# Kernel tuning notes

Measured on AMD Instinct MI355X. Metric: run time of the kernel, lower is better.

Reference implementation:

```python
import jax, jax.numpy as jnp
import numpy as np
import math

B, S, D, H = 4, 2048, 1024, 16
HD = D // H  # head dim = 64


def setup_inputs() -> dict:
    key = jax.random.key(0)
    ks = jax.random.split(key, 8)
    queries = jax.random.normal(ks[0], (B, S, D), dtype=jnp.float32)
    keys = jax.random.normal(ks[1], (B, S, D), dtype=jnp.float32)
    values = jax.random.normal(ks[2], (B, S, D), dtype=jnp.float32)
    valid_lens = jnp.maximum(jax.random.randint(ks[3], (B,), 0, S), 1).astype(jnp.int64)
    scale = 1.0 / math.sqrt(D)
    Wq = jax.random.normal(ks[4], (H, D, HD), dtype=jnp.float32) * scale
    Wk = jax.random.normal(ks[5], (H, D, HD), dtype=jnp.float32) * scale
    Wv = jax.random.normal(ks[6], (H, D, HD), dtype=jnp.float32) * scale
    Wo = jax.random.normal(ks[7], (H * HD, D), dtype=jnp.float32) * scale
    return {"queries": queries, "keys": keys, "values": values,
            "valid_lens": valid_lens, "Wq": Wq, "Wk": Wk, "Wv": Wv, "Wo": Wo}


def reference(queries, keys, values, valid_lens, Wq, Wk, Wv, Wo):
    # Per-head projections, batched over heads: [B,S,D] x [H,D,HD] -> [B,H,S,HD]
    q = jnp.einsum('bsd,hde->bhse', queries, Wq)
    k = jnp.einsum('bsd,hde->bhse', keys, Wk)
    v = jnp.einsum('bsd,hde->bhse', values, Wv)
    # Scaled dot-product scores: [B,H,S,S]
    scores = jnp.einsum('bhse,bhte->bhst', q, k) / jnp.sqrt(jnp.float32(HD))
    # Padding mask only (causal=False default in the torch forward)
    pad = jnp.arange(S)[None, :] >= valid_lens[:, None]  # [B,S] True = masked
    scores = jnp.where(pad[:, None, None, :], -jnp.inf, scores)
    attn = jax.nn.softmax(scores, axis=-1)
    out = jnp.einsum('bhst,bhte->bhse', attn, v)  # [B,H,S,HD]
    out = out.transpose(0, 2, 1, 3).reshape(q.shape[0], S, H * HD)  # concat heads
    return out @ Wo
```

## Files before the change

### kernel.cpp

```cpp
#include <hip/hip_runtime.h>
#include <hip/hip_bf16.h>

typedef __bf16 bf16;
typedef __attribute__((ext_vector_type(8))) __bf16 bf16x8;
typedef __attribute__((ext_vector_type(4))) float f32x4;

#define DEV __device__ __forceinline__

DEV float fexp2(float x) {
#if __has_builtin(__builtin_amdgcn_exp2f)
  return __builtin_amdgcn_exp2f(x);
#else
  return exp2f(x);
#endif
}

DEV void gload_lds16(const void* g, void* l) {
  __builtin_amdgcn_global_load_lds(
      (__attribute__((address_space(1))) void*)(g),
      (__attribute__((address_space(3))) void*)(l), 16, 0, 0);
}

template <int N>
DEV void waitvm() { asm volatile("s_waitcnt vmcnt(%0)" ::"n"(N) : "memory"); }
DEV void fence() { asm volatile("" ::: "memory"); }
DEV void bar() { fence(); __builtin_amdgcn_s_barrier(); fence(); }

__global__ void k_cvt_act(const float* __restrict__ q, const float* __restrict__ k,
                          const float* __restrict__ v, bf16* __restrict__ qb,
                          bf16* __restrict__ kb, bf16* __restrict__ vb) {
  const int bid = blockIdx.x;
  const int which = bid >> 12;
  const float* in = which == 0 ? q : which == 1 ? k : v;
  bf16* out = which == 0 ? qb : which == 1 ? kb : vb;
  const int i = (bid & 4095) * 256 + threadIdx.x;
  const float4* p = reinterpret_cast<const float4*>(in) + (size_t)i * 2;
  float4 a = p[0], b = p[1];
  bf16x8 o;
  o[0] = (bf16)a.x; o[1] = (bf16)a.y; o[2] = (bf16)a.z; o[3] = (bf16)a.w;
  o[4] = (bf16)b.x; o[5] = (bf16)b.y; o[6] = (bf16)b.z; o[7] = (bf16)b.w;
  *reinterpret_cast<bf16x8*>(out + (size_t)i * 8) = o;
}

__global__ void k_cvt_w(const float* __restrict__ Wq, const float* __restrict__ Wk,
                        const float* __restrict__ Wv, const float* __restrict__ Wo,
                        bf16* __restrict__ WqkvT, bf16* __restrict__ WoT) {
  const int idx = blockIdx.x * blockDim.x + threadIdx.x;
  const int which = idx >> 20, r = idx & ((1 << 20) - 1);
  if (which < 3) {
    const float* W = which == 0 ? Wq : which == 1 ? Wk : Wv;
    const int d = r & 1023, n = r >> 10;
    float val = W[((size_t)(n >> 6) << 16) + (size_t)d * 64 + (n & 63)];
    if (which == 0) val *= 0.180336880f;
    WqkvT[((size_t)which << 20) + r] = (bf16)val;
  } else {
    const int kk = r & 1023, n = r >> 10;
    WoT[r] = (bf16)Wo[(size_t)kk * 1024 + n];
  }
}

DEV void stageA(const bf16* __restrict__ Am, bf16 (*lds)[64], int k0, int tid) {
  const int wv = tid >> 6;
#pragma unroll
  for (int l = 0; l < 2; ++l) {
    const int row = l * 64 + (tid >> 3);
    const int e = (((tid & 7) ^ (row & 7)) << 3);
    gload_lds16(Am + (size_t)row * 1024 + k0 + e,
                (char*)lds + l * 8192 + wv * 1024);
  }
}
DEV void stageBh(const bf16* __restrict__ Bt, bf16 (*lds)[64], int h, int k0, int tid) {
  const int wv = tid >> 6;
#pragma unroll
  for (int l = 0; l < 2; ++l) {
    const int row = h * 128 + l * 64 + (tid >> 3);
    const int e = (((tid & 7) ^ (row & 7)) << 3);
    gload_lds16(Bt + (size_t)row * 1024 + k0 + e,
                (char*)lds + h * 16384 + l * 8192 + wv * 1024);
  }
}

DEV bf16x8 ldsfrag(const bf16 (*lds)[64], int row, int kk, int lgrp) {
  const int ch = ((kk << 2) + lgrp) ^ (row & 7);
  return *reinterpret_cast<const bf16x8*>((const char*)&lds[row][0] + (ch << 4));
}

__global__ __launch_bounds__(512, 2) void k_gemm_qkv(const bf16* __restrict__ qA,
                                                     const bf16* __restrict__ kA,
                                                     const bf16* __restrict__ vA,
                                                     const bf16* __restrict__ Wt,
                                                     bf16* __restrict__ Qh,
                                                     bf16* __restrict__ Kh,
                                                     bf16* __restrict__ Vt) {
  __shared__ __align__(16) bf16 AsB[2][128][64];
  __shared__ __align__(16) bf16 BsB[2][256][64];
  const int tid = threadIdx.x, lane = tid & 63, w = tid >> 6;
  const int lgrp = lane >> 4, lid = lane & 15;
  const int wr = w >> 2, wn = w & 3;
  const int bid0 = blockIdx.x;
  const int bid = (bid0 & 7) * 96 + (bid0 >> 3);
  const int proj = bid >> 8;
  const int local = bid & 255;
  const int mt = local >> 2, ntl = local & 3;
  const int m0 = mt * 128, n0 = ntl * 256;
  const bf16* A = proj == 0 ? qA : proj == 1 ? kA : vA;
  const bf16* Am = A + (size_t)m0 * 1024;
  const bf16* Bt = Wt + ((size_t)proj * 1024 + n0) * 1024;

  f32x4 acc[4][4] = {};
  constexpr int NT = 16;

  stageA(Am, AsB[0], 0, tid);
  stageBh(Bt, BsB[0], 0, 0, tid);
  stageBh(Bt, BsB[0], 1, 0, tid);
  stageBh(Bt, BsB[1], 0, 64, tid);
  stageBh(Bt, BsB[1], 1, 64, tid);
  waitvm<4>();
  bar();

  int cur = 0;
  for (int kt = 0; kt < NT; ++kt) {
    bf16x8 bfr[4][2], afr[2][2];
#pragma unroll
    for (int n = 0; n < 4; ++n)
#pragma unroll
      for (int kk = 0; kk < 2; ++kk)
        bfr[n][kk] = ldsfrag(BsB[cur], wn * 64 + n * 16 + lid, kk, lgrp);
#pragma unroll
    for (int mi = 0; mi < 2; ++mi)
#pragma unroll
      for (int kk = 0; kk < 2; ++kk)
        afr[mi][kk] = ldsfrag(AsB[cur], wr * 64 + mi * 16 + lid, kk, lgrp);
    if (kt + 1 < NT) stageA(Am, AsB[cur ^ 1], (kt + 1) * 64, tid);
    bar();
    __builtin_amdgcn_s_setprio(1);
#pragma unroll
    for (int mi = 0; mi < 2; ++mi)
#pragma unroll
      for (int n = 0; n < 4; ++n)
#pragma unroll
        for (int kk = 0; kk < 2; ++kk)
          acc[mi][n] = __builtin_amdgcn_mfma_f32_16x16x32_bf16(
              afr[mi][kk], bfr[n][kk], acc[mi][n], 0, 0, 0);
    __builtin_amdgcn_s_setprio(0);
    bar();
#pragma unroll
    for (int mi = 0; mi < 2; ++mi)
#pragma unroll
      for (int kk = 0; kk < 2; ++kk)
        afr[mi][kk] = ldsfrag(AsB[cur], wr * 64 + (2 + mi) * 16 + lid, kk, lgrp);
    if (kt + 2 < NT) {
      stageBh(Bt, BsB[cur], 0, (kt + 2) * 64, tid);
      stageBh(Bt, BsB[cur], 1, (kt + 2) * 64, tid);
    }
    bar();
    __builtin_amdgcn_s_setprio(1);
#pragma unroll
    for (int mi = 0; mi < 2; ++mi)
#pragma unroll
      for (int n = 0; n < 4; ++n)
#pragma unroll
        for (int kk = 0; kk < 2; ++kk)
          acc[2 + mi][n] = __builtin_amdgcn_mfma_f32_16x16x32_bf16(
              afr[mi][kk], bfr[n][kk], acc[2 + mi][n], 0, 0, 0);
    __builtin_amdgcn_s_setprio(0);
    if (kt < NT - 2) waitvm<4>();
    else if (kt == NT - 2) waitvm<0>();
    bar();
    cur ^= 1;
  }

  const int hh = (n0 >> 6) + wn;
  if (proj == 0) {
#pragma unroll
    for (int mm = 0; mm < 4; ++mm) {
      const int rowb = m0 + wr * 64 + mm * 16 + lgrp * 4;
      const int bb = rowb >> 11, s = rowb & 2047;
#pragma unroll
      for (int n = 0; n < 4; ++n) {
        const int e = n * 16 + lid;
        bf16* dst = Qh + (((size_t)bb * 16 + hh) * 2048 + s) * 64 + e;
#pragma unroll
        for (int r = 0; r < 4; ++r) dst[(size_t)r * 64] = (bf16)acc[mm][n][r];
      }
    }
  } else if (proj == 1) {
#pragma unroll
    for (int mm = 0; mm < 4; ++mm) {
      const int rowb = m0 + wr * 64 + mm * 16 + lgrp * 4;
      const int bb = rowb >> 11, s = rowb & 2047;
#pragma unroll
      for (int n = 0; n < 4; ++n) {
        const int e = n * 16 + lid;
#pragma unroll
        for (int r = 0; r < 4; ++r) {
          const int sr = s + r;
          Kh[(((size_t)bb * 16 + hh) * 2048 + sr) * 64 + (e ^ ((sr & 7) << 3))] =
              (bf16)acc[mm][n][r];
        }
      }
    }
  } else {
#pragma unroll
    for (int mm = 0; mm < 4; ++mm) {
      const int rowb = m0 + wr * 64 + mm * 16 + lgrp * 4;
      const int bb = rowb >> 11, s = rowb & 2047;
#pragma unroll
      for (int n = 0; n < 4; ++n) {
        const int e = n * 16 + lid;
        union { bf16 hv[4]; uint2 u; } tmp;
#pragma unroll
        for (int r = 0; r < 4; ++r) tmp.hv[r] = (bf16)acc[mm][n][r];
        bf16* dst = Vt + (((size_t)bb * 16 + hh) * 64 + e) * 2048 + (s ^ ((e & 7) << 3));
        *reinterpret_cast<uint2*>(dst) = tmp.u;
      }
    }
  }
}

__global__ __launch_bounds__(256) void k_gemm_out(const bf16* __restrict__ A,
                                                  const bf16* __restrict__ Bt,
                                                  float* __restrict__ C) {
  constexpr int K = 1024;
  __shared__ __align__(16) bf16 As[128 * 32];
  __shared__ __align__(16) bf16 Bs[128 * 32];
  const int tid = threadIdx.x;
  const int lane = tid & 63, w = tid >> 6;
  const int wr = w >> 1, wc = w & 1;
  const int lgrp = lane >> 4, lid = lane & 15;
  const int m0 = blockIdx.x * 128, n0 = blockIdx.y * 128;

  f32x4 acc[4][4] = {};
  const int c0 = w * 2, c1 = w * 2 + 1;
  const int bo0 = c0 * 1024 + lane * 16, bo1 = c1 * 1024 + lane * 16;
  const int r0 = bo0 >> 6, e0 = (bo0 & 63) >> 1;
  const int r1 = bo1 >> 6, e1 = (bo1 & 63) >> 1;

  for (int k0 = 0; k0 < K; k0 += 32) {
    __syncthreads();
    gload_lds16(A + (size_t)(m0 + r0) * K + k0 + e0, (char*)As + c0 * 1024);
    gload_lds16(A + (size_t)(m0 + r1) * K + k0 + e1, (char*)As + c1 * 1024);
    gload_lds16(Bt + (size_t)(n0 + r0) * K + k0 + e0, (char*)Bs + c0 * 1024);
    gload_lds16(Bt + (size_t)(n0 + r1) * K + k0 + e1, (char*)Bs + c1 * 1024);
    __syncthreads();
    bf16x8 af[4], bfv[4];
    for (int m = 0; m < 4; ++m)
      af[m] = *reinterpret_cast<const bf16x8*>(&As[(wr * 64 + m * 16 + lid) * 32 + lgrp * 8]);
    for (int n = 0; n < 4; ++n)
      bfv[n] = *reinterpret_cast<const bf16x8*>(&Bs[(wc * 64 + n * 16 + lid) * 32 + lgrp * 8]);
    for (int m = 0; m < 4; ++m)
      for (int n = 0; n < 4; ++n)
        acc[m][n] = __builtin_amdgcn_mfma_f32_16x16x32_bf16(af[m], bfv[n], acc[m][n], 0, 0, 0);
  }
  for (int m = 0; m < 4; ++m) {
    int rowb = m0 + wr * 64 + m * 16 + lgrp * 4;
    for (int n = 0; n < 4; ++n) {
      int col = n0 + wc * 64 + n * 16 + lid;
      for (int r = 0; r < 4; ++r)
        C[(size_t)(rowb + r) * 1024 + col] = acc[m][n][r];
    }
  }
}

__global__ __launch_bounds__(512) void k_flash(const bf16* __restrict__ Qh,
                                               const bf16* __restrict__ Ksw,
                                               const bf16* __restrict__ Vsw,
                                               const int* __restrict__ valid,
                                               bf16* __restrict__ Ob) {
  __shared__ __align__(16) char Ks[2][64 * 128];
  __shared__ __align__(16) char Vs[2][64 * 128];
  __shared__ __align__(16) char Plds[8][16 * 128];
  const int tid = threadIdx.x, lane = tid & 63, w = tid >> 6;
  const int lgrp = lane >> 4, lid = lane & 15;
  const int blk = blockIdx.x;
  const int qt = blk & 15, bh = blk >> 4;
  const int b = bh >> 4, h = bh & 15;
  const int s0 = qt * 128 + w * 16;
  const bf16* Qp = Qh + ((size_t)bh * 2048 + s0) * 64;
  const bf16* Kp = Ksw + (size_t)bh * 2048 * 64;
  const bf16* Vp = Vsw + (size_t)bh * 64 * 2048;
  const int vl = valid[b];
  const int nt = (vl + 63) >> 6;
  const int full = vl >> 6;

  const int srow = 8 * w + (lane >> 3), col8 = (lane & 7) * 8;

  gload_lds16(Kp + (size_t)srow * 64 + col8, &Ks[0][(8 * w) * 128]);
  gload_lds16(Vp + (size_t)srow * 2048 + col8, &Vs[0][(8 * w) * 128]);

  bf16x8 aq0 = *reinterpret_cast<const bf16x8*>(Qp + lid * 64 + lgrp * 8);
  bf16x8 aq1 = *reinterpret_cast<const bf16x8*>(Qp + lid * 64 + 32 + lgrp * 8);

  f32x4 Of[4] = {};
  float mrow = -1e30f;
  float lpart = 0.f;
  char* Pw = &Plds[w][0];
  float* PwF = (float*)Pw;
  const int pswz = (lid & 7) << 4;

  int cur = 0;
  for (int t = 0; t < nt; ++t) {
    const int t0 = t * 64;
    __syncthreads();
    if (t + 1 < nt) {
      const int t1 = t0 + 64;
      gload_lds16(Kp + (size_t)(t1 + srow) * 64 + col8, &Ks[cur ^ 1][(8 * w) * 128]);
      gload_lds16(Vp + (size_t)srow * 2048 + t1 + col8, &Vs[cur ^ 1][(8 * w) * 128]);
    }
    f32x4 sc[4] = {};
#pragma unroll
    for (int ct = 0; ct < 4; ++ct) {
      const int row = ct * 16 + lid;
      const char* kb = &Ks[cur][row * 128];
      const int msk = (row & 7) << 4;
      bf16x8 bk0 = *reinterpret_cast<const bf16x8*>(kb + ((lgrp * 16) ^ msk));
      bf16x8 bk1 = *reinterpret_cast<const bf16x8*>(kb + ((64 + lgrp * 16) ^ msk));
      sc[ct] = __builtin_amdgcn_mfma_f32_16x16x32_bf16(bk0, aq0, sc[ct], 0, 0, 0);
      sc[ct] = __builtin_amdgcn_mfma_f32_16x16x32_bf16(bk1, aq1, sc[ct], 0, 0, 0);
    }
    if (t >= full) {
#pragma unroll
      for (int ct = 0; ct < 4; ++ct)
#pragma unroll
        for (int r = 0; r < 4; ++r)
          sc[ct][r] = (t0 + ct * 16 + lgrp * 4 + r) >= vl ? -1e30f : sc[ct][r];
    }
    float vm = fmaxf(fmaxf(fmaxf(sc[0][0], sc[0][1]), fmaxf(sc[0][2], sc[0][3])),
                     fmaxf(fmaxf(sc[1][0], sc[1][1]), fmaxf(sc[1][2], sc[1][3])));
    vm = fmaxf(vm, fmaxf(fmaxf(fmaxf(sc[2][0], sc[2][1]), fmaxf(sc[2][2], sc[2][3])),
                         fmaxf(fmaxf(sc[3][0], sc[3][1]), fmaxf(sc[3][2], sc[3][3]))));
    if (__any(vm > mrow + 8.f)) {
      vm = fmaxf(vm, __shfl_xor(vm, 16));
      vm = fmaxf(vm, __shfl_xor(vm, 32));
      float mnew = fmaxf(mrow, vm);
      float scl = fexp2(mrow - mnew);
      mrow = mnew;
      lpart *= scl;
      if (lgrp == 0) PwF[lid] = scl;
      asm volatile("s_waitcnt lgkmcnt(0)" ::: "memory");
      f32x4 sq = *reinterpret_cast<const f32x4*>(PwF + lgrp * 4);
#pragma unroll
      for (int f = 0; f < 4; ++f)
#pragma unroll
        for (int r = 0; r < 4; ++r)
          Of[f][r] *= sq[r];
    }
#pragma unroll
    for (int ct = 0; ct < 4; ++ct)
#pragma unroll
      for (int r = 0; r < 4; ++r)
        sc[ct][r] = fexp2(sc[ct][r] - mrow);
#pragma unroll
    for (int ct = 0; ct < 4; ++ct) {
      union { bf16 hv[2]; unsigned int u; } p0, p1;
      p0.hv[0] = (bf16)sc[ct][0]; p0.hv[1] = (bf16)sc[ct][1];
      p1.hv[0] = (bf16)sc[ct][2]; p1.hv[1] = (bf16)sc[ct][3];
      char* base = Pw + lid * 128 + (((ct * 32 + lgrp * 8)) ^ pswz);
      *reinterpret_cast<unsigned int*>(base) = p0.u;
      *reinterpret_cast<unsigned int*>(base + 4) = p1.u;
    }
    asm volatile("s_waitcnt lgkmcnt(0)" ::: "memory");
    bf16x8 pa0 = *reinterpret_cast<const bf16x8*>(Pw + lid * 128 + ((lgrp * 16) ^ pswz));
    bf16x8 pa1 = *reinterpret_cast<const bf16x8*>(Pw + lid * 128 + ((64 + lgrp * 16) ^ pswz));
#pragma unroll
    for (int f = 0; f < 4; ++f) {
      const int row = f * 16 + lid;
      const char* vb = &Vs[cur][row * 128];
      const int msk = (row & 7) << 4;
      bf16x8 bv0 = *reinterpret_cast<const bf16x8*>(vb + ((lgrp * 16) ^ msk));
      bf16x8 bv1 = *reinterpret_cast<const bf16x8*>(vb + ((64 + lgrp * 16) ^ msk));
      Of[f] = __builtin_amdgcn_mfma_f32_16x16x32_bf16(pa0, bv0, Of[f], 0, 0, 0);
      Of[f] = __builtin_amdgcn_mfma_f32_16x16x32_bf16(pa1, bv1, Of[f], 0, 0, 0);
    }
    lpart += ((sc[0][0] + sc[0][1]) + (sc[0][2] + sc[0][3])) +
             ((sc[1][0] + sc[1][1]) + (sc[1][2] + sc[1][3])) +
             ((sc[2][0] + sc[2][1]) + (sc[2][2] + sc[2][3])) +
             ((sc[3][0] + sc[3][1]) + (sc[3][2] + sc[3][3]));
    cur ^= 1;
  }
  float l = lpart;
  l += __shfl_xor(l, 16);
  l += __shfl_xor(l, 32);
  float inv = 1.f / l;
  if (lgrp == 0) PwF[lid] = inv;
  asm volatile("s_waitcnt lgkmcnt(0)" ::: "memory");
  f32x4 invq = *reinterpret_cast<const f32x4*>(PwF + lgrp * 4);
  bf16* Op = Ob + ((size_t)b * 2048 + s0) * 1024 + h * 64;
#pragma unroll
  for (int r = 0; r < 4; ++r)
#pragma unroll
    for (int f = 0; f < 4; ++f)
      Op[(size_t)(lgrp * 4 + r) * 1024 + f * 16 + lid] = (bf16)(Of[f][r] * invq[r]);
}

extern "C" void kernel_launch(void* const* d_in, const int* in_sizes, int n_in,
                              void* d_out, int out_size, void* d_ws, size_t ws_size,
                              hipStream_t stream) {
  const float* q = (const float*)d_in[0];
  const float* k = (const float*)d_in[1];
  const float* v = (const float*)d_in[2];
  const int* vl = (const int*)d_in[3];
  const float* Wq = (const float*)d_in[4];
  const float* Wk = (const float*)d_in[5];
  const float* Wv = (const float*)d_in[6];
  const float* Wo = (const float*)d_in[7];

  char* ws = (char*)d_ws;
  const size_t SZW = (size_t)1024 * 1024 * 2;
  const size_t SZT = (size_t)8192 * 1024 * 2;
  bf16* WqkvT = (bf16*)(ws);
  bf16* WoT = (bf16*)(ws + 3 * SZW);
  bf16* Qh  = (bf16*)(ws + 4 * SZW);
  bf16* Kh  = (bf16*)(ws + 4 * SZW + SZT);
  bf16* Vt  = (bf16*)(ws + 4 * SZW + 2 * SZT);
  bf16* qb  = (bf16*)(ws + 4 * SZW + 3 * SZT);
  bf16* kb  = (bf16*)(ws + 4 * SZW + 4 * SZT);
  bf16* vb  = (bf16*)(ws + 4 * SZW + 5 * SZT);
  bf16* attnb = qb;

  k_cvt_act<<<12288, 256, 0, stream>>>(q, k, v, qb, kb, vb);
  k_cvt_w<<<16384, 256, 0, stream>>>(Wq, Wk, Wv, Wo, WqkvT, WoT);
  k_gemm_qkv<<<768, 512, 0, stream>>>(qb, kb, vb, WqkvT, Qh, Kh, Vt);
  k_flash<<<1024, 512, 0, stream>>>(Qh, Kh, Vt, vl, attnb);
  dim3 go(64, 8);
  k_gemm_out<<<go, 256, 0, stream>>>(attnb, WoT, (float*)d_out);
}
```

Measured before the change: 194.8 us.

## Reuse QKV GEMM pipeline for output projection and widen flash wave tiles

Moves the QKV projection's double-buffered, swizzled 128x256 k-loop into a shared macro and uses it for the output projection, replacing the simple 128x128 single-buffered GEMM with an 8-wave pipelined kernel. The flash attention kernel now gives each wave 32 query rows instead of 16, with 256-thread blocks, so each K/V tile loaded from LDS feeds twice as many MFMAs. The cost is more registers per wave for the doubled accumulators and possibly lower occupancy. The output GEMM also launches only 256 blocks, which may underfill the GPU.

```diff
diff --git a/kernel.cpp b/kernel.cpp
--- a/kernel.cpp
+++ b/kernel.cpp
@@ -79,11 +79,58 @@
                 (char*)lds + h * 16384 + l * 8192 + wv * 1024);
   }
 }
-
 DEV bf16x8 ldsfrag(const bf16 (*lds)[64], int row, int kk, int lgrp) {
   const int ch = ((kk << 2) + lgrp) ^ (row & 7);
   return *reinterpret_cast<const bf16x8*>((const char*)&lds[row][0] + (ch << 4));
 }
+
+#define GEMM_KLOOP(Am, Bt, acc)                                               \
+  stageA(Am, AsB[0], 0, tid);                                                 \
+  stageBh(Bt, BsB[0], 0, 0, tid);                                             \
+  stageBh(Bt, BsB[0], 1, 0, tid);                                             \
+  stageBh(Bt, BsB[1], 0, 64, tid);                                            \
+  stageBh(Bt, BsB[1], 1, 64, tid);                                            \
+  waitvm<4>();                                                                \
+  bar();                                                                      \
+  int cur = 0;                                                                \
+  for (int kt = 0; kt < NT; ++kt) {                                           \
+    bf16x8 bfr[4][2], afr[2][2];                                              \
+    _Pragma("unroll") for (int n = 0; n < 4; ++n)                             \
+        _Pragma("unroll") for (int kk = 0; kk < 2; ++kk)                      \
+            bfr[n][kk] = ldsfrag(BsB[cur], wn * 64 + n * 16 + lid, kk, lgrp); \
+    _Pragma("unroll") for (int mi = 0; mi < 2; ++mi)                          \
+        _Pragma("unroll") for (int kk = 0; kk < 2; ++kk)                      \
+            afr[mi][kk] = ldsfrag(AsB[cur], wr * 64 + mi * 16 + lid, kk, lgrp); \
+    if (kt + 1 < NT) stageA(Am, AsB[cur ^ 1], (kt + 1) * 64, tid);            \
+    bar();                                                                    \
+    __builtin_amdgcn_s_setprio(1);                                            \
+    _Pragma("unroll") for (int mi = 0; mi < 2; ++mi)                          \
+        _Pragma("unroll") for (int n = 0; n < 4; ++n)                         \
+            _Pragma("unroll") for (int kk = 0; kk < 2; ++kk)                  \
+                acc[mi][n] = __builtin_amdgcn_mfma_f32_16x16x32_bf16(         \
+                    afr[mi][kk], bfr[n][kk], acc[mi][n], 0, 0, 0);            \
+    __builtin_amdgcn_s_setprio(0);                                            \
+    bar();                                                                    \
+    _Pragma("unroll") for (int mi = 0; mi < 2; ++mi)                          \
+        _Pragma("unroll") for (int kk = 0; kk < 2; ++kk)                      \
+            afr[mi][kk] = ldsfrag(AsB[cur], wr * 64 + (2 + mi) * 16 + lid, kk, lgrp); \
+    if (kt + 2 < NT) {                                                        \
+      stageBh(Bt, BsB[cur], 0, (kt + 2) * 64, tid);                           \
+      stageBh(Bt, BsB[cur], 1, (kt + 2) * 64, tid);                           \
+    }                                                                         \
+    bar();                                                                    \
+    __builtin_amdgcn_s_setprio(1);                                            \
+    _Pragma("unroll") for (int mi = 0; mi < 2; ++mi)                          \
+        _Pragma("unroll") for (int n = 0; n < 4; ++n)                         \
+            _Pragma("unroll") for (int kk = 0; kk < 2; ++kk)                  \
+                acc[2 + mi][n] = __builtin_amdgcn_mfma_f32_16x16x32_bf16(     \
+                    afr[mi][kk], bfr[n][kk], acc[2 + mi][n], 0, 0, 0);        \
+    __builtin_amdgcn_s_setprio(0);                                            \
+    if (kt < NT - 2) waitvm<4>();                                             \
+    else if (kt == NT - 2) waitvm<0>();                                       \
+    bar();                                                                    \
+    cur ^= 1;                                                                 \
+  }
 
 __global__ __launch_bounds__(512, 2) void k_gemm_qkv(const bf16* __restrict__ qA,
                                                      const bf16* __restrict__ kA,
@@ -109,66 +156,7 @@
 
   f32x4 acc[4][4] = {};
   constexpr int NT = 16;
-
-  stageA(Am, AsB[0], 0, tid);
-  stageBh(Bt, BsB[0], 0, 0, tid);
-  stageBh(Bt, BsB[0], 1, 0, tid);
-  stageBh(Bt, BsB[1], 0, 64, tid);
-  stageBh(Bt, BsB[1], 1, 64, tid);
-  waitvm<4>();
-  bar();
-
-  int cur = 0;
-  for (int kt = 0; kt < NT; ++kt) {
-    bf16x8 bfr[4][2], afr[2][2];
-#pragma unroll
-    for (int n = 0; n < 4; ++n)
-#pragma unroll
-      for (int kk = 0; kk < 2; ++kk)
-        bfr[n][kk] = ldsfrag(BsB[cur], wn * 64 + n * 16 + lid, kk, lgrp);
-#pragma unroll
-    for (int mi = 0; mi < 2; ++mi)
-#pragma unroll
-      for (int kk = 0; kk < 2; ++kk)
-        afr[mi][kk] = ldsfrag(AsB[cur], wr * 64 + mi * 16 + lid, kk, lgrp);
-    if (kt + 1 < NT) stageA(Am, AsB[cur ^ 1], (kt + 1) * 64, tid);
-    bar();
-    __builtin_amdgcn_s_setprio(1);
-#pragma unroll
-    for (int mi = 0; mi < 2; ++mi)
-#pragma unroll
-      for (int n = 0; n < 4; ++n)
-#pragma unroll
-        for (int kk = 0; kk < 2; ++kk)
-          acc[mi][n] = __builtin_amdgcn_mfma_f32_16x16x32_bf16(
-              afr[mi][kk], bfr[n][kk], acc[mi][n], 0, 0, 0);
-    __builtin_amdgcn_s_setprio(0);
-    bar();
-#pragma unroll
-    for (int mi = 0; mi < 2; ++mi)
-#pragma unroll
-      for (int kk = 0; kk < 2; ++kk)
-        afr[mi][kk] = ldsfrag(AsB[cur], wr * 64 + (2 + mi) * 16 + lid, kk, lgrp);
-    if (kt + 2 < NT) {
-      stageBh(Bt, BsB[cur], 0, (kt + 2) * 64, tid);
-      stageBh(Bt, BsB[cur], 1, (kt + 2) * 64, tid);
-    }
-    bar();
-    __builtin_amdgcn_s_setprio(1);
-#pragma unroll
-    for (int mi = 0; mi < 2; ++mi)
-#pragma unroll
-      for (int n = 0; n < 4; ++n)
-#pragma unroll
-        for (int kk = 0; kk < 2; ++kk)
-          acc[2 + mi][n] = __builtin_amdgcn_mfma_f32_16x16x32_bf16(
-              afr[mi][kk], bfr[n][kk], acc[2 + mi][n], 0, 0, 0);
-    __builtin_amdgcn_s_setprio(0);
-    if (kt < NT - 2) waitvm<4>();
-    else if (kt == NT - 2) waitvm<0>();
-    bar();
-    cur ^= 1;
-  }
+  GEMM_KLOOP(Am, Bt, acc)
 
   const int hh = (n0 >> 6) + wn;
   if (proj == 0) {
@@ -218,64 +206,52 @@
   }
 }
 
-__global__ __launch_bounds__(256) void k_gemm_out(const bf16* __restrict__ A,
-                                                  const bf16* __restrict__ Bt,
-                                                  float* __restrict__ C) {
-  constexpr int K = 1024;
-  __shared__ __align__(16) bf16 As[128 * 32];
-  __shared__ __align__(16) bf16 Bs[128 * 32];
-  const int tid = threadIdx.x;
-  const int lane = tid & 63, w = tid >> 6;
-  const int wr = w >> 1, wc = w & 1;
+__global__ __launch_bounds__(512, 2) void k_gemm_out8(const bf16* __restrict__ A,
+                                                      const bf16* __restrict__ Wo,
+                                                      float* __restrict__ C) {
+  __shared__ __align__(16) bf16 AsB[2][128][64];
+  __shared__ __align__(16) bf16 BsB[2][256][64];
+  const int tid = threadIdx.x, lane = tid & 63, w = tid >> 6;
   const int lgrp = lane >> 4, lid = lane & 15;
-  const int m0 = blockIdx.x * 128, n0 = blockIdx.y * 128;
+  const int wr = w >> 2, wn = w & 3;
+  const int bid0 = blockIdx.x;
+  const int bid = (bid0 & 7) * 32 + (bid0 >> 3);
+  const int mt = bid >> 2, ntl = bid & 3;
+  const int m0 = mt * 128, n0 = ntl * 256;
+  const bf16* Am = A + (size_t)m0 * 1024;
+  const bf16* Bt = Wo + (size_t)n0 * 1024;
 
   f32x4 acc[4][4] = {};
-  const int c0 = w * 2, c1 = w * 2 + 1;
-  const int bo0 = c0 * 1024 + lane * 16, bo1 = c1 * 1024 + lane * 16;
-  const int r0 = bo0 >> 6, e0 = (bo0 & 63) >> 1;
-  const int r1 = bo1 >> 6, e1 = (bo1 & 63) >> 1;
-
-  for (int k0 = 0; k0 < K; k0 += 32) {
-    __syncthreads();
-    gload_lds16(A + (size_t)(m0 + r0) * K + k0 + e0, (char*)As + c0 * 1024);
-    gload_lds16(A + (size_t)(m0 + r1) * K + k0 + e1, (char*)As + c1 * 1024);
-    gload_lds16(Bt + (size_t)(n0 + r0) * K + k0 + e0, (char*)Bs + c0 * 1024);
-    gload_lds16(Bt + (size_t)(n0 + r1) * K + k0 + e1, (char*)Bs + c1 * 1024);
-    __syncthreads();
-    bf16x8 af[4], bfv[4];
-    for (int m = 0; m < 4; ++m)
-      af[m] = *reinterpret_cast<const bf16x8*>(&As[(wr * 64 + m * 16 + lid) * 32 + lgrp * 8]);
-    for (int n = 0; n < 4; ++n)
-      bfv[n] = *reinterpret_cast<const bf16x8*>(&Bs[(wc * 64 + n * 16 + lid) * 32 + lgrp * 8]);
-    for (int m = 0; m < 4; ++m)
-      for (int n = 0; n < 4; ++n)
-        acc[m][n] = __builtin_amdgcn_mfma_f32_16x16x32_bf16(af[m], bfv[n], acc[m][n], 0, 0, 0);
-  }
-  for (int m = 0; m < 4; ++m) {
-    int rowb = m0 + wr * 64 + m * 16 + lgrp * 4;
+  constexpr int NT = 16;
+  GEMM_KLOOP(Am, Bt, acc)
+
+#pragma unroll
+  for (int mm = 0; mm < 4; ++mm) {
+    const int rowb = m0 + wr * 64 + mm * 16 + lgrp * 4;
+#pragma unroll
     for (int n = 0; n < 4; ++n) {
-      int col = n0 + wc * 64 + n * 16 + lid;
+      const int col = n0 + wn * 64 + n * 16 + lid;
+#pragma unroll
       for (int r = 0; r < 4; ++r)
-        C[(size_t)(rowb + r) * 1024 + col] = acc[m][n][r];
-    }
-  }
-}
-
-__global__ __launch_bounds__(512) void k_flash(const bf16* __restrict__ Qh,
-                                               const bf16* __restrict__ Ksw,
-                                               const bf16* __restrict__ Vsw,
-                                               const int* __restrict__ valid,
-                                               bf16* __restrict__ Ob) {
-  __shared__ __align__(16) char Ks[2][64 * 128];
-  __shared__ __align__(16) char Vs[2][64 * 128];
-  __shared__ __align__(16) char Plds[8][16 * 128];
+        C[(size_t)(rowb + r) * 1024 + col] = acc[mm][n][r];
+    }
+  }
+}
+
+__global__ __launch_bounds__(256, 3) void k_flash(const bf16* __restrict__ Qh,
+                                                  const bf16* __restrict__ Ksw,
+                                                  const bf16* __restrict__ Vsw,
+                                                  const int* __restrict__ valid,
+                                                  bf16* __restrict__ Ob) {
+  __shared__ __align__(16) char Ks[2][8192];
+  __shared__ __align__(16) char Vs[2][8192];
+  __shared__ __align__(16) char Plds[4][4096];
   const int tid = threadIdx.x, lane = tid & 63, w = tid >> 6;
   const int lgrp = lane >> 4, lid = lane & 15;
   const int blk = blockIdx.x;
   const int qt = blk & 15, bh = blk >> 4;
   const int b = bh >> 4, h = bh & 15;
-  const int s0 = qt * 128 + w * 16;
+  const int s0 = qt * 128 + w * 32;
   const bf16* Qp = Qh + ((size_t)bh * 2048 + s0) * 64;
   const bf16* Kp = Ksw + (size_t)bh * 2048 * 64;
   const bf16* Vp = Vsw + (size_t)bh * 64 * 2048;
@@ -283,17 +259,23 @@
   const int nt = (vl + 63) >> 6;
   const int full = vl >> 6;
 
-  const int srow = 8 * w + (lane >> 3), col8 = (lane & 7) * 8;
-
-  gload_lds16(Kp + (size_t)srow * 64 + col8, &Ks[0][(8 * w) * 128]);
-  gload_lds16(Vp + (size_t)srow * 2048 + col8, &Vs[0][(8 * w) * 128]);
-
-  bf16x8 aq0 = *reinterpret_cast<const bf16x8*>(Qp + lid * 64 + lgrp * 8);
-  bf16x8 aq1 = *reinterpret_cast<const bf16x8*>(Qp + lid * 64 + 32 + lgrp * 8);
-
-  f32x4 Of[4] = {};
-  float mrow = -1e30f;
-  float lpart = 0.f;
+  const int sr0 = 16 * w + (lane >> 3), col8 = (lane & 7) * 8;
+
+  gload_lds16(Kp + (size_t)sr0 * 64 + col8, &Ks[0][(16 * w) * 128]);
+  gload_lds16(Kp + (size_t)(sr0 + 8) * 64 + col8, &Ks[0][(16 * w + 8) * 128]);
+  gload_lds16(Vp + (size_t)sr0 * 2048 + col8, &Vs[0][(16 * w) * 128]);
+  gload_lds16(Vp + (size_t)(sr0 + 8) * 2048 + col8, &Vs[0][(16 * w + 8) * 128]);
+
+  bf16x8 aq[2][2];
+#pragma unroll
+  for (int g = 0; g < 2; ++g)
+#pragma unroll
+    for (int c = 0; c < 2; ++c)
+      aq[g][c] = *reinterpret_cast<const bf16x8*>(Qp + (g * 16 + lid) * 64 + c * 32 + lgrp * 8);
+
+  f32x4 Of[2][4] = {};
+  float mrow[2] = {-1e30f, -1e30f};
+  float lpart[2] = {0.f, 0.f};
   char* Pw = &Plds[w][0];
   float* PwF = (float*)Pw;
   const int pswz = (lid & 7) << 4;
@@ -304,64 +286,95 @@
     __syncthreads();
     if (t + 1 < nt) {
       const int t1 = t0 + 64;
-      gload_lds16(Kp + (size_t)(t1 + srow) * 64 + col8, &Ks[cur ^ 1][(8 * w) * 128]);
-      gload_lds16(Vp + (size_t)srow * 2048 + t1 + col8, &Vs[cur ^ 1][(8 * w) * 128]);
-    }
-    f32x4 sc[4] = {};
-#pragma unroll
-    for (int ct = 0; ct < 4; ++ct) {
-      const int row = ct * 16 + lid;
-      const char* kb = &Ks[cur][row * 128];
-      const int msk = (row & 7) << 4;
-      bf16x8 bk0 = *reinterpret_cast<const bf16x8*>(kb + ((lgrp * 16) ^ msk));
-      bf16x8 bk1 = *reinterpret_cast<const bf16x8*>(kb + ((64 + lgrp * 16) ^ msk));
-      sc[ct] = __builtin_amdgcn_mfma_f32_16x16x32_bf16(bk0, aq0, sc[ct], 0, 0, 0);
-      sc[ct] = __builtin_amdgcn_mfma_f32_16x16x32_bf16(bk1, aq1, sc[ct], 0, 0, 0);
+      gload_lds16(Kp + (size_t)(t1 + sr0) * 64 + col8, &Ks[cur ^ 1][(16 * w) * 128]);
+      gload_lds16(Kp + (size_t)(t1 + sr0 + 8) * 64 + col8, &Ks[cur ^ 1][(16 * w + 8) * 128]);
+      gload_lds16(Vp + (size_t)sr0 * 2048 + t1 + col8, &Vs[cur ^ 1][(16 * w) * 128]);
+      gload_lds16(Vp + (size_t)(sr0 + 8) * 2048 + t1 + col8, &Vs[cur ^ 1][(16 * w + 8) * 128]);
+    }
+    f32x4 sc[2][4] = {{}, {}};
+#pragma unroll
+    for (int kk = 0; kk < 2; ++kk) {
+      bf16x8 bkh[4];
+#pragma unroll
+      for (int ct = 0; ct < 4; ++ct) {
+        const int row = ct * 16 + lid;
+        bkh[ct] = *reinterpret_cast<const bf16x8*>(
+            &Ks[cur][row * 128] + ((kk * 64 + lgrp * 16) ^ ((row & 7) << 4)));
+      }
+#pragma unroll
+      for (int g = 0; g < 2; ++g)
+#pragma unroll
+        for (int ct = 0; ct < 4; ++ct)
+          sc[g][ct] = __builtin_amdgcn_mfma_f32_16x16x32_bf16(bkh[ct], aq[g][kk],
+                                                              sc[g][ct], 0, 0, 0);
     }
     if (t >= full) {
 #pragma unroll
       for (int ct = 0; ct < 4; ++ct)
 #pragma unroll
+        for (int r = 0; r < 4; ++r) {
+          const bool m = (t0 + ct * 16 + lgrp * 4 + r) >= vl;
+          sc[0][ct][r] = m ? -1e30f : sc[0][ct][r];
+          sc[1][ct][r] = m ? -1e30f : sc[1][ct][r];
+        }
+    }
+    float vm[2];
+#pragma unroll
+    for (int g = 0; g < 2; ++g) {
+      float v = fmaxf(fmaxf(fmaxf(sc[g][0][0], sc[g][0][1]), fmaxf(sc[g][0][2], sc[g][0][3])),
+                      fmaxf(fmaxf(sc[g][1][0], sc[g][1][1]), fmaxf(sc[g][1][2], sc[g][1][3])));
+      v = fmaxf(v, fmaxf(fmaxf(fmaxf(sc[g][2][0], sc[g][2][1]), fmaxf(sc[g][2][2], sc[g][2][3])),
+                         fmaxf(fmaxf(sc[g][3][0], sc[g][3][1]), fmaxf(sc[g][3][2], sc[g][3][3]))));
+      vm[g] = v;
+    }
+    if (__any((vm[0] > mrow[0] + 8.f) | (vm[1] > mrow[1] + 8.f))) {
+#pragma unroll
+      for (int g = 0; g < 2; ++g) {
+        float v = vm[g];
+        v = fmaxf(v, __shfl_xor(v, 16));
+        v = fmaxf(v, __shfl_xor(v, 32));
+        float mnew = fmaxf(mrow[g], v);
+        float scl = fexp2(mrow[g] - mnew);
+        mrow[g] = mnew;
+        lpart[g] *= scl;
+        if (lgrp == 0) PwF[g * 512 + lid] = scl;
+      }
+      asm volatile("s_waitcnt lgkmcnt(0)" ::: "memory");
+      f32x4 sq0 = *reinterpret_cast<const f32x4*>(PwF + lgrp * 4);
+      f32x4 sq1 = *reinterpret_cast<const f32x4*>(PwF + 512 + lgrp * 4);
+#pragma unroll
+      for (int f = 0; f < 4; ++f)
+#pragma unroll
+        for (int r = 0; r < 4; ++r) {
+          Of[0][f][r] *= sq0[r];
+          Of[1][f][r] *= sq1[r];
+        }
+    }
+#pragma unroll
+    for (int g = 0; g < 2; ++g)
+#pragma unroll
+      for (int ct = 0; ct < 4; ++ct)
+#pragma unroll
         for (int r = 0; r < 4; ++r)
-          sc[ct][r] = (t0 + ct * 16 + lgrp * 4 + r) >= vl ? -1e30f : sc[ct][r];
-    }
-    float vm = fmaxf(fmaxf(fmaxf(sc[0][0], sc[0][1]), fmaxf(sc[0][2], sc[0][3])),
-                     fmaxf(fmaxf(sc[1][0], sc[1][1]), fmaxf(sc[1][2], sc[1][3])));
-    vm = fmaxf(vm, fmaxf(fmaxf(fmaxf(sc[2][0], sc[2][1]), fmaxf(sc[2][2], sc[2][3])),
-                         fmaxf(fmaxf(sc[3][0], sc[3][1]), fmaxf(sc[3][2], sc[3][3]))));
-    if (__any(vm > mrow + 8.f)) {
-      vm = fmaxf(vm, __shfl_xor(vm, 16));
-      vm = fmaxf(vm, __shfl_xor(vm, 32));
-      float mnew = fmaxf(mrow, vm);
-      float scl = fexp2(mrow - mnew);
-      mrow = mnew;
-      lpart *= scl;
-      if (lgrp == 0) PwF[lid] = scl;
-      asm volatile("s_waitcnt lgkmcnt(0)" ::: "memory");
-      f32x4 sq = *reinterpret_cast<const f32x4*>(PwF + lgrp * 4);
-#pragma unroll
-      for (int f = 0; f < 4; ++f)
-#pragma unroll
-        for (int r = 0; r < 4; ++r)
-          Of[f][r] *= sq[r];
-    }
-#pragma unroll
-    for (int ct = 0; ct < 4; ++ct)
-#pragma unroll
-      for (int r = 0; r < 4; ++r)
-        sc[ct][r] = fexp2(sc[ct][r] - mrow);
-#pragma unroll
-    for (int ct = 0; ct < 4; ++ct) {
-      union { bf16 hv[2]; unsigned int u; } p0, p1;
-      p0.hv[0] = (bf16)sc[ct][0]; p0.hv[1] = (bf16)sc[ct][1];
-      p1.hv[0] = (bf16)sc[ct][2]; p1.hv[1] = (bf16)sc[ct][3];
-      char* base = Pw + lid * 128 + (((ct * 32 + lgrp * 8)) ^ pswz);
-      *reinterpret_cast<unsigned int*>(base) = p0.u;
-      *reinterpret_cast<unsigned int*>(base + 4) = p1.u;
-    }
+          sc[g][ct][r] = fexp2(sc[g][ct][r] - mrow[g]);
+#pragma unroll
+    for (int g = 0; g < 2; ++g)
+#pragma unroll
+      for (int ct = 0; ct < 4; ++ct) {
+        union { bf16 hv[2]; unsigned int u; } p0, p1;
+        p0.hv[0] = (bf16)sc[g][ct][0]; p0.hv[1] = (bf16)sc[g][ct][1];
+        p1.hv[0] = (bf16)sc[g][ct][2]; p1.hv[1] = (bf16)sc[g][ct][3];
+        char* base = Pw + g * 2048 + lid * 128 + ((ct * 32 + lgrp * 8) ^ pswz);
+        *reinterpret_cast<unsigned int*>(base) = p0.u;
+        *reinterpret_cast<unsigned int*>(base + 4) = p1.u;
+      }
     asm volatile("s_waitcnt lgkmcnt(0)" ::: "memory");
-    bf16x8 pa0 = *reinterpret_cast<const bf16x8*>(Pw + lid * 128 + ((lgrp * 16) ^ pswz));
-    bf16x8 pa1 = *reinterpret_cast<const bf16x8*>(Pw + lid * 128 + ((64 + lgrp * 16) ^ pswz));
+    bf16x8 pa[2][2];
+#pragma unroll
+    for (int g = 0; g < 2; ++g) {
+      pa[g][0] = *reinterpret_cast<const bf16x8*>(Pw + g * 2048 + lid * 128 + ((lgrp * 16) ^ pswz));
+      pa[g][1] = *reinterpret_cast<const bf16x8*>(Pw + g * 2048 + lid * 128 + ((64 + lgrp * 16) ^ pswz));
+    }
 #pragma unroll
     for (int f = 0; f < 4; ++f) {
       const int row = f * 16 + lid;
@@ -369,28 +382,37 @@
       const int msk = (row & 7) << 4;
       bf16x8 bv0 = *reinterpret_cast<const bf16x8*>(vb + ((lgrp * 16) ^ msk));
       bf16x8 bv1 = *reinterpret_cast<const bf16x8*>(vb + ((64 + lgrp * 16) ^ msk));
-      Of[f] = __builtin_amdgcn_mfma_f32_16x16x32_bf16(pa0, bv0, Of[f], 0, 0, 0);
-      Of[f] = __builtin_amdgcn_mfma_f32_16x16x32_bf16(pa1, bv1, Of[f], 0, 0, 0);
-    }
-    lpart += ((sc[0][0] + sc[0][1]) + (sc[0][2] + sc[0][3])) +
-             ((sc[1][0] + sc[1][1]) + (sc[1][2] + sc[1][3])) +
-             ((sc[2][0] + sc[2][1]) + (sc[2][2] + sc[2][3])) +
-             ((sc[3][0] + sc[3][1]) + (sc[3][2] + sc[3][3]));
+      Of[0][f] = __builtin_amdgcn_mfma_f32_16x16x32_bf16(pa[0][0], bv0, Of[0][f], 0, 0, 0);
+      Of[0][f] = __builtin_amdgcn_mfma_f32_16x16x32_bf16(pa[0][1], bv1, Of[0][f], 0, 0, 0);
+      Of[1][f] = __builtin_amdgcn_mfma_f32_16x16x32_bf16(pa[1][0], bv0, Of[1][f], 0, 0, 0);
+      Of[1][f] = __builtin_amdgcn_mfma_f32_16x16x32_bf16(pa[1][1], bv1, Of[1][f], 0, 0, 0);
+    }
+#pragma unroll
+    for (int g = 0; g < 2; ++g)
+      lpart[g] += ((sc[g][0][0] + sc[g][0][1]) + (sc[g][0][2] + sc[g][0][3])) +
+                  ((sc[g][1][0] + sc[g][1][1]) + (sc[g][1][2] + sc[g][1][3])) +
+                  ((sc[g][2][0] + sc[g][2][1]) + (sc[g][2][2] + sc[g][2][3])) +
+                  ((sc[g][3][0] + sc[g][3][1]) + (sc[g][3][2] + sc[g][3][3]));
     cur ^= 1;
   }
-  float l = lpart;
-  l += __shfl_xor(l, 16);
-  l += __shfl_xor(l, 32);
-  float inv = 1.f / l;
-  if (lgrp == 0) PwF[lid] = inv;
+#pragma unroll
+  for (int g = 0; g < 2; ++g) {
+    float l = lpart[g];
+    l += __shfl_xor(l, 16);
+    l += __shfl_xor(l, 32);
+    if (lgrp == 0) PwF[g * 512 + lid] = 1.f / l;
+  }
   asm volatile("s_waitcnt lgkmcnt(0)" ::: "memory");
-  f32x4 invq = *reinterpret_cast<const f32x4*>(PwF + lgrp * 4);
+  f32x4 iq0 = *reinterpret_cast<const f32x4*>(PwF + lgrp * 4);
+  f32x4 iq1 = *reinterpret_cast<const f32x4*>(PwF + 512 + lgrp * 4);
   bf16* Op = Ob + ((size_t)b * 2048 + s0) * 1024 + h * 64;
 #pragma unroll
   for (int r = 0; r < 4; ++r)
 #pragma unroll
-    for (int f = 0; f < 4; ++f)
-      Op[(size_t)(lgrp * 4 + r) * 1024 + f * 16 + lid] = (bf16)(Of[f][r] * invq[r]);
+    for (int f = 0; f < 4; ++f) {
+      Op[(size_t)(lgrp * 4 + r) * 1024 + f * 16 + lid] = (bf16)(Of[0][f][r] * iq0[r]);
+      Op[(size_t)(16 + lgrp * 4 + r) * 1024 + f * 16 + lid] = (bf16)(Of[1][f][r] * iq1[r]);
+    }
 }
 
 extern "C" void kernel_launch(void* const* d_in, const int* in_sizes, int n_in,
@@ -421,7 +443,6 @@
   k_cvt_act<<<12288, 256, 0, stream>>>(q, k, v, qb, kb, vb);
   k_cvt_w<<<16384, 256, 0, stream>>>(Wq, Wk, Wv, Wo, WqkvT, WoT);
   k_gemm_qkv<<<768, 512, 0, stream>>>(qb, kb, vb, WqkvT, Qh, Kh, Vt);
-  k_flash<<<1024, 512, 0, stream>>>(Qh, Kh, Vt, vl, attnb);
-  dim3 go(64, 8);
-  k_gemm_out<<<go, 256, 0, stream>>>(attnb, WoT, (float*)d_out);
-}
+  k_flash<<<1024, 256, 0, stream>>>(Qh, Kh, Vt, vl, attnb);
+  k_gemm_out8<<<256, 512, 0, stream>>>(attnb, WoT, (float*)d_out);
+}
```

New measurement: 181.4 us. -6.9%, faster.
